# Kernel tuning notes

Measured on AMD Instinct MI355X. Metric: run time of the kernel, lower is better.

Reference implementation:

```python
import jax, jax.numpy as jnp
import numpy as np

D = 512   # dim (number of groups)
H = 8192  # h = dim * v
U = 64    # u
V = H // D  # 16
N = 4096  # batch
EPS = 1e-12  # torch F.normalize eps


def setup_inputs() -> dict:
    key = jax.random.key(0)
    k_x, k_w1, k_b1, k_w2, k_b2 = jax.random.split(key, 5)
    x = jax.random.normal(k_x, (N, H), dtype=jnp.float32)
    # grouped Conv1d(dim*v, dim*u, k=1, groups=dim) == per-group [u, v] matmul
    s1 = 1.0 / np.sqrt(V)
    W1 = jax.random.uniform(k_w1, (D, U, V), jnp.float32, -s1, s1)
    b1 = jax.random.uniform(k_b1, (D, U), jnp.float32, -s1, s1)
    # grouped Conv1d(dim*u, dim, k=1, groups=dim) == per-group [1, u] matmul
    s2 = 1.0 / np.sqrt(U)
    W2 = jax.random.uniform(k_w2, (D, U), jnp.float32, -s2, s2)
    b2 = jax.random.uniform(k_b2, (D,), jnp.float32, -s2, s2)
    return {"x": x, "W1": W1, "b1": b1, "W2": W2, "b2": b2}


def reference(x, W1, b1, W2, b2):
    # x: [N, H] -> [N, D, V] (channel layout of Conv1d groups)
    xg = x.reshape(-1, D, V)
    # grouped 1x1 conv #1: per-group v -> u matmul, + bias
    h1 = jnp.einsum('ndv,duv->ndu', xg, W1) + b1  # [N, D, U]
    h1 = jax.nn.elu(h1)
    # grouped 1x1 conv #2: per-group u -> 1 matmul, + bias
    y = jnp.einsum('ndu,du->nd', h1, W2) + b2  # [N, D]
    # L2 normalize (torch F.normalize semantics: x / max(||x||, eps))
    nrm = jnp.sqrt(jnp.sum(y * y, axis=-1, keepdims=True))
    return y / jnp.maximum(nrm, EPS)
```

## Files before the change

kernel.cpp:

```cpp
#include <hip/hip_runtime.h>
#include <math.h>

#define D_ 512
#define H_ 8192
#define U_ 64
#define V_ 16
#define N_ 4096

#define BR 32
#define BG 16
#define XPAD 4
#define XSTR (BG * V_ + XPAD)

typedef __bf16 bf16x8 __attribute__((ext_vector_type(8)));
typedef float f32x4 __attribute__((ext_vector_type(4)));

__global__ __launch_bounds__(256) void k1_div_encoder(
        const float* __restrict__ x,
        const float* __restrict__ W1,
        const float* __restrict__ b1,
        const float* __restrict__ W2,
        const float* __restrict__ b2,
        float* __restrict__ y) {
    __shared__ float xs[BR][XSTR];
    __shared__ float ytile[BR][BG + 1];

    const int tid  = threadIdx.x;
    const int lane = tid & 63;
    const int wave = __builtin_amdgcn_readfirstlane(tid >> 6);
    const int q    = lane >> 4;
    const int m    = lane & 15;
    const int vbase = (q & 1) * 8;

    const int nb = blockIdx.x & 127;
    const int db = blockIdx.x >> 7;
    const int r0 = nb * BR;
    const int d0 = db * BG;

    {
        const float* xg = x + (size_t)r0 * H_ + (size_t)d0 * V_;
        #pragma unroll
        for (int i = 0; i < 8; ++i) {
            const int flat = tid + i * 256;
            const int row  = flat >> 6;
            const int c4   = flat & 63;
            f32x4 v = *(const f32x4*)(xg + (size_t)row * H_ + c4 * 4);
            *(f32x4*)&xs[row][c4 * 4] = v;
        }
    }
    __syncthreads();

    for (int gi = 0; gi < 4; ++gi) {
        const int gl = wave * 4 + gi;
        const int d  = d0 + gl;

        bf16x8 Afrag[4];
        #pragma unroll
        for (int c = 0; c < 4; ++c) {
            const float* wp = W1 + ((size_t)d * U_ + c * 16 + m) * V_ + vbase;
            f32x4 w0 = *(const f32x4*)wp;
            f32x4 w1v = *(const f32x4*)(wp + 4);
            float wf[8] = {w0.x, w0.y, w0.z, w0.w, w1v.x, w1v.y, w1v.z, w1v.w};
            bf16x8 a;
            if (q < 2) {
                #pragma unroll
                for (int i = 0; i < 8; ++i) a[i] = (__bf16)wf[i];
            } else {
                #pragma unroll
                for (int i = 0; i < 8; ++i) {
                    __bf16 h = (__bf16)wf[i];
                    a[i] = (__bf16)(wf[i] - (float)h);
                }
            }
            Afrag[c] = a;
        }
        f32x4 b1frag[4], w2frag[4];
        #pragma unroll
        for (int c = 0; c < 4; ++c) {
            b1frag[c] = *(const f32x4*)(b1 + (size_t)d * U_ + c * 16 + q * 4);
            w2frag[c] = *(const f32x4*)(W2 + (size_t)d * U_ + c * 16 + q * 4);
        }
        const float b2s = b2[d];

        #pragma unroll
        for (int t = 0; t < 2; ++t) {
            const float* bp = &xs[t * 16 + m][gl * V_ + vbase];
            f32x4 x0 = *(const f32x4*)bp;
            f32x4 x1 = *(const f32x4*)(bp + 4);
            float xf[8] = {x0.x, x0.y, x0.z, x0.w, x1.x, x1.y, x1.z, x1.w};
            bf16x8 bhi, blo;
            #pragma unroll
            for (int i = 0; i < 8; ++i) {
                __bf16 h = (__bf16)xf[i];
                bhi[i] = h;
                blo[i] = (__bf16)(xf[i] - (float)h);
            }

            float partial = 0.0f;
            #pragma unroll
            for (int c = 0; c < 4; ++c) {
                f32x4 acc = b1frag[c];
                acc = __builtin_amdgcn_mfma_f32_16x16x32_bf16(Afrag[c], bhi, acc, 0, 0, 0);
                acc = __builtin_amdgcn_mfma_f32_16x16x32_bf16(Afrag[c], blo, acc, 0, 0, 0);
                #pragma unroll
                for (int r = 0; r < 4; ++r) {
                    float h = acc[r];
                    float e = (h > 0.0f) ? h : (__expf(h) - 1.0f);
                    partial = fmaf(w2frag[c][r], e, partial);
                }
            }
            partial += __shfl_xor(partial, 16, 64);
            partial += __shfl_xor(partial, 32, 64);
            if (q == 0) {
                ytile[t * 16 + m][gl] = partial + b2s;
            }
        }
    }
    __syncthreads();

    if (tid < 128) {
        const int row = tid >> 2;
        const int c4  = (tid & 3) * 4;
        f32x4 v;
        v.x = ytile[row][c4 + 0];
        v.y = ytile[row][c4 + 1];
        v.z = ytile[row][c4 + 2];
        v.w = ytile[row][c4 + 3];
        *(f32x4*)(y + (size_t)(r0 + row) * D_ + d0 + c4) = v;
    }
}

__global__ __launch_bounds__(256) void k2_l2_normalize(float* __restrict__ y) {
    const int n = blockIdx.x;
    const int t = threadIdx.x;
    float* row = y + (size_t)n * D_;

    float v0 = row[t];
    float v1 = row[t + 256];
    float ss = v0 * v0 + v1 * v1;

    #pragma unroll
    for (int off = 32; off > 0; off >>= 1) {
        ss += __shfl_down(ss, off, 64);
    }

    __shared__ float wsum[4];
    if ((t & 63) == 0) wsum[t >> 6] = ss;
    __syncthreads();
    const float tot = wsum[0] + wsum[1] + wsum[2] + wsum[3];

    const float scale = 1.0f / fmaxf(sqrtf(tot), 1e-12f);

    row[t]       = v0 * scale;
    row[t + 256] = v1 * scale;
}

extern "C" void kernel_launch(void* const* d_in, const int* in_sizes, int n_in,
                              void* d_out, int out_size, void* d_ws, size_t ws_size,
                              hipStream_t stream) {
    const float* x  = (const float*)d_in[0];
    const float* W1 = (const float*)d_in[1];
    const float* b1 = (const float*)d_in[2];
    const float* W2 = (const float*)d_in[3];
    const float* b2 = (const float*)d_in[4];
    float* y = (float*)d_out;

    k1_div_encoder<<<dim3((N_ / BR) * (D_ / BG)), dim3(256), 0, stream>>>(
        x, W1, b1, W2, b2, y);
    k2_l2_normalize<<<dim3(N_), dim3(256), 0, stream>>>(y);
}
```

Before: 256.3 us.

## Pre-split W1 into bf16 hi/lo and retile encoder to 64 rows by 8 groups

Adds a pre-pass kernel that splits W1 once into bf16 high and low halves in workspace, so the main kernel loads ready-made MFMA fragments instead of converting fp32 weights in every block. The encoder tile changes from 32x16 to 64x8 (rows x groups), so each weight fragment is reused across four row sub-tiles instead of two. It also adds a launch-bounds occupancy hint, a branchless ELU, and a vectorized y-tile store. The cost is an extra kernel launch, plus workspace traffic for the split weights, and the path depends on the workspace being large enough.

```diff
diff --git a/kernel.cpp b/kernel.cpp
--- a/kernel.cpp
+++ b/kernel.cpp
@@ -6,24 +6,45 @@
 #define U_ 64
 #define V_ 16
 #define N_ 4096
-
-#define BR 32
-#define BG 16
-#define XPAD 4
-#define XSTR (BG * V_ + XPAD)
+#define DUV (D_ * U_ * V_)
+
+#define BR 64
+#define BG 8
+#define XSTR (BG * V_ + 4)
+#define YSTR 12
 
 typedef __bf16 bf16x8 __attribute__((ext_vector_type(8)));
+typedef __bf16 bf16x4 __attribute__((ext_vector_type(4)));
 typedef float f32x4 __attribute__((ext_vector_type(4)));
 
-__global__ __launch_bounds__(256) void k1_div_encoder(
+__global__ __launch_bounds__(256) void k0_split_w1(const float* __restrict__ W1,
+                                                   __bf16* __restrict__ wh) {
+    __bf16* wl = wh + DUV;
+    const int i4 = (blockIdx.x * 256 + threadIdx.x) * 4;
+    f32x4 w = *(const f32x4*)(W1 + i4);
+    bf16x4 h, l;
+    #pragma unroll
+    for (int j = 0; j < 4; ++j) {
+        float wf = w[j];
+        __bf16 hh = (__bf16)wf;
+        h[j] = hh;
+        l[j] = (__bf16)(wf - (float)hh);
+    }
+    *(bf16x4*)(wh + i4) = h;
+    *(bf16x4*)(wl + i4) = l;
+}
+
+template <bool PRESPLIT>
+__global__ __launch_bounds__(256, 4) void k1_div_encoder(
         const float* __restrict__ x,
         const float* __restrict__ W1,
+        const __bf16* __restrict__ wsplit,
         const float* __restrict__ b1,
         const float* __restrict__ W2,
         const float* __restrict__ b2,
         float* __restrict__ y) {
     __shared__ float xs[BR][XSTR];
-    __shared__ float ytile[BR][BG + 1];
+    __shared__ float ytile[BR][YSTR];
 
     const int tid  = threadIdx.x;
     const int lane = tid & 63;
@@ -32,8 +53,8 @@
     const int m    = lane & 15;
     const int vbase = (q & 1) * 8;
 
-    const int nb = blockIdx.x & 127;
-    const int db = blockIdx.x >> 7;
+    const int nb = blockIdx.x & 63;
+    const int db = blockIdx.x >> 6;
     const int r0 = nb * BR;
     const int d0 = db * BG;
 
@@ -42,38 +63,45 @@
         #pragma unroll
         for (int i = 0; i < 8; ++i) {
             const int flat = tid + i * 256;
-            const int row  = flat >> 6;
-            const int c4   = flat & 63;
+            const int row  = flat >> 5;
+            const int c4   = flat & 31;
             f32x4 v = *(const f32x4*)(xg + (size_t)row * H_ + c4 * 4);
             *(f32x4*)&xs[row][c4 * 4] = v;
         }
     }
     __syncthreads();
 
-    for (int gi = 0; gi < 4; ++gi) {
-        const int gl = wave * 4 + gi;
+    #pragma unroll 1
+    for (int gi = 0; gi < 2; ++gi) {
+        const int gl = wave * 2 + gi;
         const int d  = d0 + gl;
 
         bf16x8 Afrag[4];
-        #pragma unroll
-        for (int c = 0; c < 4; ++c) {
-            const float* wp = W1 + ((size_t)d * U_ + c * 16 + m) * V_ + vbase;
-            f32x4 w0 = *(const f32x4*)wp;
-            f32x4 w1v = *(const f32x4*)(wp + 4);
-            float wf[8] = {w0.x, w0.y, w0.z, w0.w, w1v.x, w1v.y, w1v.z, w1v.w};
-            bf16x8 a;
-            if (q < 2) {
-                #pragma unroll
-                for (int i = 0; i < 8; ++i) a[i] = (__bf16)wf[i];
-            } else {
+        if (PRESPLIT) {
+            const __bf16* base = wsplit + (size_t)(q >> 1) * DUV;
+            #pragma unroll
+            for (int c = 0; c < 4; ++c) {
+                Afrag[c] = *(const bf16x8*)(base +
+                    ((size_t)d * U_ + c * 16 + m) * V_ + vbase);
+            }
+        } else {
+            #pragma unroll
+            for (int c = 0; c < 4; ++c) {
+                const float* wp = W1 + ((size_t)d * U_ + c * 16 + m) * V_ + vbase;
+                f32x4 w0 = *(const f32x4*)wp;
+                f32x4 w1v = *(const f32x4*)(wp + 4);
+                float wf[8] = {w0.x, w0.y, w0.z, w0.w, w1v.x, w1v.y, w1v.z, w1v.w};
+                bf16x8 a;
                 #pragma unroll
                 for (int i = 0; i < 8; ++i) {
                     __bf16 h = (__bf16)wf[i];
-                    a[i] = (__bf16)(wf[i] - (float)h);
+                    __bf16 l = (__bf16)(wf[i] - (float)h);
+                    a[i] = (q < 2) ? h : l;
                 }
-            }
-            Afrag[c] = a;
-        }
+                Afrag[c] = a;
+            }
+        }
+
         f32x4 b1frag[4], w2frag[4];
         #pragma unroll
         for (int c = 0; c < 4; ++c) {
@@ -82,8 +110,8 @@
         }
         const float b2s = b2[d];
 
-        #pragma unroll
-        for (int t = 0; t < 2; ++t) {
+        #pragma unroll 2
+        for (int t = 0; t < 4; ++t) {
             const float* bp = &xs[t * 16 + m][gl * V_ + vbase];
             f32x4 x0 = *(const f32x4*)bp;
             f32x4 x1 = *(const f32x4*)(bp + 4);
@@ -105,7 +133,7 @@
                 #pragma unroll
                 for (int r = 0; r < 4; ++r) {
                     float h = acc[r];
-                    float e = (h > 0.0f) ? h : (__expf(h) - 1.0f);
+                    float e = fmaxf(h, __expf(fminf(h, 0.0f)) - 1.0f);
                     partial = fmaf(w2frag[c][r], e, partial);
                 }
             }
@@ -119,14 +147,10 @@
     __syncthreads();
 
     if (tid < 128) {
-        const int row = tid >> 2;
-        const int c4  = (tid & 3) * 4;
-        f32x4 v;
-        v.x = ytile[row][c4 + 0];
-        v.y = ytile[row][c4 + 1];
-        v.z = ytile[row][c4 + 2];
-        v.w = ytile[row][c4 + 3];
-        *(f32x4*)(y + (size_t)(r0 + row) * D_ + d0 + c4) = v;
+        const int row  = tid >> 1;
+        const int half = tid & 1;
+        f32x4 v = *(const f32x4*)&ytile[row][half * 4];
+        *(f32x4*)(y + (size_t)(r0 + row) * D_ + d0 + half * 4) = v;
     }
 }
 
@@ -165,7 +189,15 @@
     const float* b2 = (const float*)d_in[4];
     float* y = (float*)d_out;
 
-    k1_div_encoder<<<dim3((N_ / BR) * (D_ / BG)), dim3(256), 0, stream>>>(
-        x, W1, b1, W2, b2, y);
+    const dim3 grid((N_ / BR) * (D_ / BG));
+    if (ws_size >= (size_t)(2 * DUV * sizeof(__bf16))) {
+        __bf16* wh = (__bf16*)d_ws;
+        k0_split_w1<<<dim3(DUV / 4 / 256), dim3(256), 0, stream>>>(W1, wh);
+        k1_div_encoder<true><<<grid, dim3(256), 0, stream>>>(
+            x, W1, wh, b1, W2, b2, y);
+    } else {
+        k1_div_encoder<false><<<grid, dim3(256), 0, stream>>>(
+            x, W1, (const __bf16*)nullptr, b1, W2, b2, y);
+    }
     k2_l2_normalize<<<dim3(N_), dim3(256), 0, stream>>>(y);
 }
```

Result: faster. 220.6 us (-13.9%).
